# Kernel tuning notes

Measured on AMD Instinct MI355X. Metric: run time of the kernel, lower is better.

Reference implementation:

```python
import jax, jax.numpy as jnp
import numpy as np

B, C, N, K_NN = 16, 64, 2048, 3
OUT_C = 64


def setup_inputs() -> dict:
    key = jax.random.key(0)
    k1, k2, k3 = jax.random.split(key, 3)
    x = jax.random.normal(k1, (B, C, N), dtype=jnp.float32)
    fan_in = C * K_NN
    bound = 1.0 / np.sqrt(fan_in)
    W = jax.random.uniform(k2, (OUT_C, C, K_NN), minval=-bound, maxval=bound, dtype=jnp.float32)
    b = jax.random.uniform(k3, (OUT_C,), minval=-bound, maxval=bound, dtype=jnp.float32)
    return {"x": x, "W": W, "b": b}


def reference(x, W, b):
    # x: [B, C, N]; W: [O, C, K]; b: [O]
    K = W.shape[-1]
    # Pairwise squared distances: dist[b,i,j] = |x_i|^2 + |x_j|^2 - 2 x_i.x_j.
    # The original takes sqrt, but sqrt is monotone and the distances are only
    # used for top-k index selection, so we select on squared distances (same indices).
    norm_sq = jnp.sum(x * x, axis=1)                      # [B, N]
    dot = jnp.einsum('bcn,bcm->bnm', x, x)                # [B, N, N]
    dist_sq = norm_sq[:, :, None] + norm_sq[:, None, :] - 2.0 * dot  # [B, N, N]
    # K smallest distances per row -> neighbor indices [B, N, K]
    _, idx = jax.lax.top_k(-dist_sq, K)
    # Gather neighbors: neigh[b, c, n, k] = x[b, c, idx[b, n, k]]
    neigh = jax.vmap(lambda xb, ib: xb[:, ib])(x, idx)    # [B, C, N, K]
    # Conv1d with kernel_size == stride == K over the flattened [B, C, N*K]
    # tensor is exactly a per-window contraction over the K neighbors.
    out = jnp.einsum('bcnk,ock->bon', neigh, W) + b[None, :, None]  # [B, O, N]
    return out
```

## Files before the change

kernel.cpp:

```cpp
#include <hip/hip_runtime.h>
#include <cfloat>
#include <climits>

#define B_DIM 16
#define C_DIM 64
#define N_DIM 2048
#define O_DIM 64
#define K_NN  3

typedef __attribute__((ext_vector_type(8))) short bf16x8;
typedef __attribute__((ext_vector_type(4))) float floatx4;

#define GLDS16(gsrc, ldst)                                        \
  __builtin_amdgcn_global_load_lds(                               \
      (const __attribute__((address_space(1))) void*)(gsrc),      \
      (__attribute__((address_space(3))) void*)(ldst), 16, 0, 0)

__device__ __forceinline__ unsigned short f32_to_bf16_rne(float f) {
  unsigned int u = __float_as_uint(f);
  return (unsigned short)((u + 0x7fffu + ((u >> 16) & 1u)) >> 16);
}
__device__ __forceinline__ float bf16_to_f32(unsigned short h) {
  return __uint_as_float(((unsigned int)h) << 16);
}

__device__ __forceinline__ unsigned med3u(unsigned a, unsigned b, unsigned c) {
  unsigned mn = min(a, b), mx = max(a, b);
  return max(mn, min(mx, c));
}

__device__ __forceinline__ void ins4p(unsigned u, int jv, unsigned* k, int* j) {
  bool c3 = u < k[3], c2 = u < k[2], c1 = u < k[1], c0 = u < k[0];
  k[3] = c2 ? k[2] : (c3 ? u  : k[3]);
  j[3] = c2 ? j[2] : (c3 ? jv : j[3]);
  k[2] = c1 ? k[1] : (c2 ? u  : k[2]);
  j[2] = c1 ? j[1] : (c2 ? jv : j[2]);
  k[1] = c0 ? k[0] : (c1 ? u  : k[1]);
  j[1] = c0 ? j[0] : (c1 ? jv : j[1]);
  k[0] = c0 ? u  : k[0];
  j[0] = c0 ? jv : j[0];
}

__global__ __launch_bounds__(256) void prep_kernel(
    const float* __restrict__ x, float* __restrict__ xT,
    unsigned short* __restrict__ xTh, unsigned short* __restrict__ xTl,
    double* __restrict__ nd, float* __restrict__ nf,
    const float* __restrict__ W, float* __restrict__ Wt) {
  int bid = blockIdx.x;
  int t = threadIdx.x;
  if (bid >= 512) {
    int t2 = (bid - 512) * 256 + t;
    int o  = t2 / (C_DIM * K_NN);
    int ck = t2 - o * (C_DIM * K_NN);
    Wt[ck * O_DIM + o] = W[t2];
    return;
  }
  __shared__ __align__(16) float xs[C_DIM][68];
  int b  = bid >> 5;
  int n0 = (bid & 31) * 64;
  const float* xb = x + (size_t)b * C_DIM * N_DIM;
  #pragma unroll
  for (int r = 0; r < 4; ++r) {
    int idx = r * 256 + t;
    int c = idx >> 4;
    int qq = idx & 15;
    *(float4*)&xs[c][qq * 4] = *(const float4*)(xb + (size_t)c * N_DIM + n0 + qq * 4);
  }
  __syncthreads();
  int n = t >> 2, cg = t & 3;
  float v[16];
  #pragma unroll
  for (int cc = 0; cc < 16; ++cc) v[cc] = xs[cg * 16 + cc][n];
  double ps = 0.0;
  #pragma unroll
  for (int cc = 0; cc < 16; ++cc) ps = fma((double)v[cc], (double)v[cc], ps);
  ps += __shfl_xor(ps, 1, 64);
  ps += __shfl_xor(ps, 2, 64);
  size_t row = (size_t)b * N_DIM + n0 + n;
  #pragma unroll
  for (int qq = 0; qq < 4; ++qq) {
    float4 wv; wv.x = v[qq*4]; wv.y = v[qq*4+1]; wv.z = v[qq*4+2]; wv.w = v[qq*4+3];
    *(float4*)&xT[row * C_DIM + cg * 16 + qq * 4] = wv;
  }
  unsigned short hh[16], ll[16];
  #pragma unroll
  for (int cc = 0; cc < 16; ++cc) {
    hh[cc] = f32_to_bf16_rne(v[cc]);
    ll[cc] = f32_to_bf16_rne(v[cc] - bf16_to_f32(hh[cc]));
  }
  #pragma unroll
  for (int e = 0; e < 2; ++e) {
    int phys = (2 * cg + e) ^ (n & 7);
    unsigned int hp[4], lp[4];
    #pragma unroll
    for (int xk = 0; xk < 4; ++xk) {
      hp[xk] = (unsigned)hh[e*8 + 2*xk] | ((unsigned)hh[e*8 + 2*xk + 1] << 16);
      lp[xk] = (unsigned)ll[e*8 + 2*xk] | ((unsigned)ll[e*8 + 2*xk + 1] << 16);
    }
    ((uint4*)xTh)[row * 8 + phys] = *(uint4*)hp;
    ((uint4*)xTl)[row * 8 + phys] = *(uint4*)lp;
  }
  if (cg == 0) {
    nd[row] = ps;
    nf[row] = (float)ps + 512.0f;
  }
}

__global__ __launch_bounds__(256, 4) void topk_kernel(
    const unsigned short* __restrict__ xTh, const unsigned short* __restrict__ xTl,
    const float* __restrict__ nf, unsigned short* __restrict__ cand) {
  __shared__ __align__(16) unsigned short Jh[2][64 * 64];
  __shared__ __align__(16) unsigned short Jl[2][64 * 64];
  int bid   = blockIdx.x;
  int q     = bid & 3;
  int itile = (bid >> 2) & 15;
  int b     = bid >> 6;
  int i0    = itile * 128;
  int jq0   = q * 512;
  int t = threadIdx.x;
  int w = t >> 6, lane = t & 63, quad = lane >> 4, col = lane & 15;
  int csw = col & 7;
  const unsigned short* xh = xTh + (size_t)b * N_DIM * 64;
  const unsigned short* xl = xTl + (size_t)b * N_DIM * 64;
  const float* nfb = nf + b * N_DIM;

  bf16x8 ih[2][2], il[2][2];
  #pragma unroll
  for (int s2 = 0; s2 < 2; ++s2) {
    #pragma unroll
    for (int ks = 0; ks < 2; ++ks) {
      size_t row = i0 + w * 32 + s2 * 16 + col;
      int phys = (ks * 4 + quad) ^ csw;
      ih[s2][ks] = *(const bf16x8*)(xh + row * 64 + phys * 8);
      il[s2][ks] = *(const bf16x8*)(xl + row * 64 + phys * 8);
    }
  }

  unsigned ck[2][4];
  #pragma unroll
  for (int s2 = 0; s2 < 2; ++s2)
    ck[s2][0] = ck[s2][1] = ck[s2][2] = ck[s2][3] = 0xFFFFFFFFu;

  int a0 = col * 64 + ((quad ^ csw) * 8);
  int a1 = col * 64 + (((4 + quad) ^ csw) * 8);

  const unsigned short* sbh = xh + (size_t)(jq0 + w * 16) * 64 + lane * 8;
  const unsigned short* sbl = xl + (size_t)(jq0 + w * 16) * 64 + lane * 8;
  int ldsb = w * 16 * 64;

  #pragma unroll
  for (int k2 = 0; k2 < 2; ++k2) {
    GLDS16(sbh + k2 * 512, &Jh[0][ldsb + k2 * 512]);
    GLDS16(sbl + k2 * 512, &Jl[0][ldsb + k2 * 512]);
  }
  __syncthreads();

  #pragma unroll
  for (int js = 0; js < 8; ++js) {
    int cur = js & 1, nxt = cur ^ 1;
    int j0 = jq0 + js * 64;

    if (js < 7) {
      #pragma unroll
      for (int k2 = 0; k2 < 2; ++k2) {
        GLDS16(sbh + (js + 1) * 4096 + k2 * 512, &Jh[nxt][ldsb + k2 * 512]);
        GLDS16(sbl + (js + 1) * 4096 + k2 * 512, &Jl[nxt][ldsb + k2 * 512]);
      }
    }

    floatx4 acc[2][4];
    #pragma unroll
    for (int s2 = 0; s2 < 2; ++s2)
      #pragma unroll
      for (int jt = 0; jt < 4; ++jt) acc[s2][jt] = (floatx4){0.f, 0.f, 0.f, 0.f};

    #pragma unroll
    for (int ks = 0; ks < 2; ++ks) {
      int ab = ks ? a1 : a0;
      #pragma unroll
      for (int jt = 0; jt < 4; ++jt) {
        bf16x8 jh = *(const bf16x8*)&Jh[cur][jt * 1024 + ab];
        bf16x8 jl = *(const bf16x8*)&Jl[cur][jt * 1024 + ab];
        #pragma unroll
        for (int s2 = 0; s2 < 2; ++s2) {
          acc[s2][jt] = __builtin_amdgcn_mfma_f32_16x16x32_bf16(jl, ih[s2][ks], acc[s2][jt], 0, 0, 0);
          acc[s2][jt] = __builtin_amdgcn_mfma_f32_16x16x32_bf16(jh, il[s2][ks], acc[s2][jt], 0, 0, 0);
          acc[s2][jt] = __builtin_amdgcn_mfma_f32_16x16x32_bf16(jh, ih[s2][ks], acc[s2][jt], 0, 0, 0);
        }
      }
    }

    unsigned locb = (unsigned)(js << 4);
    int jb = j0 + quad * 4;
    #pragma unroll
    for (int jt = 0; jt < 4; ++jt) {
      float4 nv = *(const float4*)(nfb + jb + jt * 16);
      float nfa[4] = {nv.x, nv.y, nv.z, nv.w};
      #pragma unroll
      for (int r = 0; r < 4; ++r) {
        unsigned idbits = locb | (unsigned)(jt * 4 + r);
        #pragma unroll
        for (int s2 = 0; s2 < 2; ++s2) {
          float key = fmaf(-2.0f, acc[s2][jt][r], nfa[r]);
          unsigned u = (__float_as_uint(key) & 0xFFFFFF80u) | idbits;
          unsigned m0 = min(ck[s2][0], u);
          unsigned m1 = med3u(ck[s2][0], u, ck[s2][1]);
          unsigned m2 = med3u(ck[s2][1], u, ck[s2][2]);
          unsigned m3 = med3u(ck[s2][2], u, ck[s2][3]);
          ck[s2][0] = m0; ck[s2][1] = m1; ck[s2][2] = m2; ck[s2][3] = m3;
        }
      }
    }

    __syncthreads();
  }

  #pragma unroll
  for (int s2 = 0; s2 < 2; ++s2) {
    int cj[4];
    unsigned cku[4];
    #pragma unroll
    for (int s = 0; s < 4; ++s) {
      unsigned loc = ck[s2][s] & 127u;
      cj[s] = jq0 + (int)((loc >> 4) << 6) + (int)(((loc >> 2) & 3u) << 4) +
              (quad << 2) + (int)(loc & 3u);
      cku[s] = ck[s2][s];
    }
    #pragma unroll
    for (int m = 16; m < 64; m <<= 1) {
      unsigned tu[4]; int tj[4];
      #pragma unroll
      for (int s = 0; s < 4; ++s) {
        tu[s] = __shfl_xor(cku[s], m, 64);
        tj[s] = __shfl_xor(cj[s], m, 64);
      }
      #pragma unroll
      for (int s = 0; s < 4; ++s) ins4p(tu[s], tj[s], cku, cj);
    }
    if (quad == 0) {
      int row = b * N_DIM + i0 + w * 32 + s2 * 16 + col;
      unsigned short* cp = cand + row * 16 + q * 4;
      cp[0] = (unsigned short)cj[0];
      cp[1] = (unsigned short)cj[1];
      cp[2] = (unsigned short)cj[2];
      cp[3] = (unsigned short)cj[3];
    }
  }
}

#define NT   64
#define NPAD 68
__global__ __launch_bounds__(256) void conv_kernel(
    const float* __restrict__ xT, const double* __restrict__ nd,
    const unsigned short* __restrict__ cand,
    const float* __restrict__ Wt, const float* __restrict__ bias,
    float* __restrict__ out) {
  __shared__ __align__(16) float nb[C_DIM * K_NN][NPAD];
  __shared__ unsigned short tks[NT][4];
  int bid = blockIdx.x;
  int b  = bid >> 5;
  int n0 = (bid & 31) * NT;
  const float* xtb = xT + (size_t)b * N_DIM * C_DIM;
  int t = threadIdx.x;
  int w = t >> 6, lane = t & 63;
  int cid = lane >> 2, seg = lane & 3;

  for (int it = 0; it < 16; ++it) {
    int nn = w * 16 + it;
    int row = b * N_DIM + n0 + nn;
    int j = cand[row * 16 + cid];
    const float* xn = xtb + ((size_t)(n0 + nn) * C_DIM) + seg * 16;
    const float* xj = xtb + ((size_t)j * C_DIM) + seg * 16;
    double pd = 0.0;
    #pragma unroll
    for (int qq = 0; qq < 4; ++qq) {
      float4 a  = *(const float4*)(xn + qq * 4);
      float4 bb = *(const float4*)(xj + qq * 4);
      pd = fma((double)a.x, (double)bb.x, pd);
      pd = fma((double)a.y, (double)bb.y, pd);
      pd = fma((double)a.z, (double)bb.z, pd);
      pd = fma((double)a.w, (double)bb.w, pd);
    }
    pd += __shfl_xor(pd, 1, 64);
    pd += __shfl_xor(pd, 2, 64);
    double key = fma(-2.0, pd, nd[b * N_DIM + j] + 512.0);
    unsigned long long u =
        ((unsigned long long)__double_as_longlong(key) & ~2047ull) |
        (unsigned long long)(unsigned)j;
    unsigned long long v = u;
    #pragma unroll
    for (int p = 0; p < 3; ++p) {
      unsigned long long m = v;
      #pragma unroll
      for (int msk = 4; msk < 64; msk <<= 1) {
        unsigned long long o = __shfl_xor(m, msk, 64);
        m = (o < m) ? o : m;
      }
      if (lane == 0) tks[nn][p] = (unsigned short)(m & 2047ull);
      v = (v == m) ? ~0ull : v;
    }
  }
  __syncthreads();

  #pragma unroll
  for (int p = 0; p < 12; ++p) {
    int u = p * 256 + t;
    int sg = u & 15;
    int r  = u >> 4;
    int k = r >> 6, n = r & 63;
    int j = tks[n][k];
    float4 v = *(const float4*)(xtb + (size_t)j * C_DIM + sg * 4);
    nb[(sg * 4 + 0) * 3 + k][n] = v.x;
    nb[(sg * 4 + 1) * 3 + k][n] = v.y;
    nb[(sg * 4 + 2) * 3 + k][n] = v.z;
    nb[(sg * 4 + 3) * 3 + k][n] = v.w;
  }
  __syncthreads();

  int ng = t & 15, og = t >> 4;
  float acc[4][4];
  #pragma unroll
  for (int oo = 0; oo < 4; ++oo) {
    float bv = bias[(og << 2) + oo];
    #pragma unroll
    for (int nn2 = 0; nn2 < 4; ++nn2) acc[oo][nn2] = bv;
  }
  const float* nbp = &nb[0][0] + (ng << 2);
  const float* wtp = Wt + (og << 2);
  #pragma unroll 4
  for (int ckk = 0; ckk < C_DIM * K_NN; ++ckk) {
    float4 nv = *(const float4*)(nbp + ckk * NPAD);
    float4 wv = *(const float4*)(wtp + ckk * O_DIM);
    float na[4] = {nv.x, nv.y, nv.z, nv.w};
    float wa[4] = {wv.x, wv.y, wv.z, wv.w};
    #pragma unroll
    for (int oo = 0; oo < 4; ++oo)
      #pragma unroll
      for (int nn2 = 0; nn2 < 4; ++nn2)
        acc[oo][nn2] = fmaf(wa[oo], na[nn2], acc[oo][nn2]);
  }
  #pragma unroll
  for (int oo = 0; oo < 4; ++oo) {
    int o = (og << 2) + oo;
    float4 v; v.x = acc[oo][0]; v.y = acc[oo][1]; v.z = acc[oo][2]; v.w = acc[oo][3];
    *(float4*)&out[(size_t)(b * O_DIM + o) * N_DIM + n0 + (ng << 2)] = v;
  }
}

extern "C" void kernel_launch(void* const* d_in, const int* in_sizes, int n_in,
                              void* d_out, int out_size, void* d_ws, size_t ws_size,
                              hipStream_t stream) {
  const float* x    = (const float*)d_in[0];
  const float* W    = (const float*)d_in[1];
  const float* bias = (const float*)d_in[2];
  float* out = (float*)d_out;
  char* ws = (char*)d_ws;
  float*          xT  = (float*)ws;
  unsigned short* xTh = (unsigned short*)(ws + 8388608);
  unsigned short* xTl = (unsigned short*)(ws + 12582912);
  double*         nd  = (double*)(ws + 16777216);
  float*          nfp = (float*)(ws + 17039360);
  unsigned short* cd  = (unsigned short*)(ws + 17170432);
  float*          Wt  = (float*)(ws + 18219008);

  prep_kernel<<<512 + 48, 256, 0, stream>>>(x, xT, xTh, xTl, nd, nfp, W, Wt);
  topk_kernel<<<B_DIM * 16 * 4, 256, 0, stream>>>(xTh, xTl, nfp, cd);
  conv_kernel<<<B_DIM * (N_DIM / NT), 256, 0, stream>>>(xT, nd, cd, Wt, bias, out);
}
```

Measured before the change: 144.6 us.

## Shrink conv tile to 16 points per block for more blocks

```diff
diff --git a/kernel.cpp b/kernel.cpp
--- a/kernel.cpp
+++ b/kernel.cpp
@@ -248,9 +248,9 @@
   }
 }
 
-#define NT   64
-#define NPAD 68
-__global__ __launch_bounds__(256) void conv_kernel(
+#define NT   16
+#define NPAD 20
+__global__ __launch_bounds__(256, 6) void conv_kernel(
     const float* __restrict__ xT, const double* __restrict__ nd,
     const unsigned short* __restrict__ cand,
     const float* __restrict__ Wt, const float* __restrict__ bias,
@@ -258,15 +258,15 @@
   __shared__ __align__(16) float nb[C_DIM * K_NN][NPAD];
   __shared__ unsigned short tks[NT][4];
   int bid = blockIdx.x;
-  int b  = bid >> 5;
-  int n0 = (bid & 31) * NT;
+  int b  = bid >> 7;
+  int n0 = (bid & 127) * NT;
   const float* xtb = xT + (size_t)b * N_DIM * C_DIM;
   int t = threadIdx.x;
   int w = t >> 6, lane = t & 63;
   int cid = lane >> 2, seg = lane & 3;
 
-  for (int it = 0; it < 16; ++it) {
-    int nn = w * 16 + it;
+  for (int it = 0; it < 4; ++it) {
+    int nn = w * 4 + it;
     int row = b * N_DIM + n0 + nn;
     int j = cand[row * 16 + cid];
     const float* xn = xtb + ((size_t)(n0 + nn) * C_DIM) + seg * 16;
@@ -303,11 +303,12 @@
   __syncthreads();
 
   #pragma unroll
-  for (int p = 0; p < 12; ++p) {
+  for (int p = 0; p < 3; ++p) {
     int u = p * 256 + t;
-    int sg = u & 15;
-    int r  = u >> 4;
-    int k = r >> 6, n = r & 63;
+    int n  = u & 15;
+    int h  = u >> 4;
+    int k  = h >> 4;
+    int sg = h & 15;
     int j = tks[n][k];
     float4 v = *(const float4*)(xtb + (size_t)j * C_DIM + sg * 4);
     nb[(sg * 4 + 0) * 3 + k][n] = v.x;
@@ -317,34 +318,26 @@
   }
   __syncthreads();
 
-  int ng = t & 15, og = t >> 4;
-  float acc[4][4];
-  #pragma unroll
-  for (int oo = 0; oo < 4; ++oo) {
-    float bv = bias[(og << 2) + oo];
-    #pragma unroll
-    for (int nn2 = 0; nn2 < 4; ++nn2) acc[oo][nn2] = bv;
+  int ng = t & 3, og = t >> 2;
+  float acc[4];
+  {
+    float bv = bias[og];
+    #pragma unroll
+    for (int nn2 = 0; nn2 < 4; ++nn2) acc[nn2] = bv;
   }
   const float* nbp = &nb[0][0] + (ng << 2);
-  const float* wtp = Wt + (og << 2);
-  #pragma unroll 4
+  const float* wtp = Wt + og;
+  #pragma unroll 8
   for (int ckk = 0; ckk < C_DIM * K_NN; ++ckk) {
     float4 nv = *(const float4*)(nbp + ckk * NPAD);
-    float4 wv = *(const float4*)(wtp + ckk * O_DIM);
-    float na[4] = {nv.x, nv.y, nv.z, nv.w};
-    float wa[4] = {wv.x, wv.y, wv.z, wv.w};
-    #pragma unroll
-    for (int oo = 0; oo < 4; ++oo)
-      #pragma unroll
-      for (int nn2 = 0; nn2 < 4; ++nn2)
-        acc[oo][nn2] = fmaf(wa[oo], na[nn2], acc[oo][nn2]);
-  }
-  #pragma unroll
-  for (int oo = 0; oo < 4; ++oo) {
-    int o = (og << 2) + oo;
-    float4 v; v.x = acc[oo][0]; v.y = acc[oo][1]; v.z = acc[oo][2]; v.w = acc[oo][3];
-    *(float4*)&out[(size_t)(b * O_DIM + o) * N_DIM + n0 + (ng << 2)] = v;
-  }
+    float wv = wtp[ckk * O_DIM];
+    acc[0] = fmaf(wv, nv.x, acc[0]);
+    acc[1] = fmaf(wv, nv.y, acc[1]);
+    acc[2] = fmaf(wv, nv.z, acc[2]);
+    acc[3] = fmaf(wv, nv.w, acc[3]);
+  }
+  float4 v; v.x = acc[0]; v.y = acc[1]; v.z = acc[2]; v.w = acc[3];
+  *(float4*)&out[(size_t)(b * O_DIM + og) * N_DIM + n0 + (ng << 2)] = v;
 }
 
 extern "C" void kernel_launch(void* const* d_in, const int* in_sizes, int n_in,
```

After: 140.5 us. -2.8%, faster.

## Split exact top-k refinement into separate kernel and remap block order by XCD

Applied to the files above, without the earlier changes.

```diff
diff --git a/kernel.cpp b/kernel.cpp
--- a/kernel.cpp
+++ b/kernel.cpp
@@ -112,6 +112,7 @@
   __shared__ __align__(16) unsigned short Jh[2][64 * 64];
   __shared__ __align__(16) unsigned short Jl[2][64 * 64];
   int bid   = blockIdx.x;
+  bid = (bid & 7) * 128 + (bid >> 3);
   int q     = bid & 3;
   int itile = (bid >> 2) & 15;
   int b     = bid >> 6;
@@ -248,72 +249,91 @@
   }
 }
 
+#define RNT 16
+__global__ __launch_bounds__(256, 4) void refine_kernel(
+    const float* __restrict__ xT, const double* __restrict__ nd,
+    const unsigned short* __restrict__ cand,
+    unsigned long long* __restrict__ tks_g) {
+  __shared__ unsigned long long keys[RNT][17];
+  int bid = blockIdx.x;
+  bid = (bid & 7) * 256 + (bid >> 3);
+  int b  = bid >> 7;
+  int n0 = (bid & 127) * RNT;
+  int t = threadIdx.x;
+  int row = t >> 4, c = t & 15;
+  int nn = n0 + row;
+  int j = cand[(b * N_DIM + nn) * 16 + c];
+  const float* xtb = xT + (size_t)b * N_DIM * C_DIM;
+  const float* xn = xtb + (size_t)nn * C_DIM;
+  const float* xj = xtb + (size_t)j * C_DIM;
+  double nj = nd[b * N_DIM + j];
+
+  double p[4];
+  #pragma unroll
+  for (int qq = 0; qq < 4; ++qq) {
+    double s = 0.0;
+    #pragma unroll
+    for (int r = 0; r < 4; ++r) {
+      float4 a  = *(const float4*)(xn + qq * 16 + r * 4);
+      float4 bb = *(const float4*)(xj + qq * 16 + r * 4);
+      s = fma((double)a.x, (double)bb.x, s);
+      s = fma((double)a.y, (double)bb.y, s);
+      s = fma((double)a.z, (double)bb.z, s);
+      s = fma((double)a.w, (double)bb.w, s);
+    }
+    p[qq] = s;
+  }
+  double pd = (p[0] + p[1]) + (p[2] + p[3]);
+  double key = fma(-2.0, pd, nj + 512.0);
+  unsigned long long u =
+      ((unsigned long long)__double_as_longlong(key) & ~2047ull) |
+      (unsigned long long)(unsigned)j;
+  keys[row][c] = u;
+  __syncthreads();
+
+  if (t < RNT) {
+    unsigned long long k0 = ~0ull, k1 = ~0ull, k2 = ~0ull;
+    #pragma unroll
+    for (int s = 0; s < 16; ++s) {
+      unsigned long long v = keys[t][s];
+      bool c0 = v < k0, c1 = v < k1, c2 = v < k2;
+      k2 = c1 ? k1 : (c2 ? v : k2);
+      k1 = c0 ? k0 : (c1 ? v : k1);
+      k0 = c0 ? v : k0;
+    }
+    tks_g[b * N_DIM + n0 + t] =
+        (k0 & 2047ull) | ((k1 & 2047ull) << 16) | ((k2 & 2047ull) << 32);
+  }
+}
+
 #define NT   64
 #define NPAD 68
-__global__ __launch_bounds__(256) void conv_kernel(
-    const float* __restrict__ xT, const double* __restrict__ nd,
-    const unsigned short* __restrict__ cand,
+__global__ __launch_bounds__(256, 2) void conv_kernel(
+    const float* __restrict__ xT, const unsigned long long* __restrict__ tks_g,
     const float* __restrict__ Wt, const float* __restrict__ bias,
     float* __restrict__ out) {
   __shared__ __align__(16) float nb[C_DIM * K_NN][NPAD];
-  __shared__ unsigned short tks[NT][4];
   int bid = blockIdx.x;
+  bid = (bid & 7) * 64 + (bid >> 3);
   int b  = bid >> 5;
   int n0 = (bid & 31) * NT;
   const float* xtb = xT + (size_t)b * N_DIM * C_DIM;
   int t = threadIdx.x;
   int w = t >> 6, lane = t & 63;
-  int cid = lane >> 2, seg = lane & 3;
-
-  for (int it = 0; it < 16; ++it) {
-    int nn = w * 16 + it;
-    int row = b * N_DIM + n0 + nn;
-    int j = cand[row * 16 + cid];
-    const float* xn = xtb + ((size_t)(n0 + nn) * C_DIM) + seg * 16;
-    const float* xj = xtb + ((size_t)j * C_DIM) + seg * 16;
-    double pd = 0.0;
-    #pragma unroll
-    for (int qq = 0; qq < 4; ++qq) {
-      float4 a  = *(const float4*)(xn + qq * 4);
-      float4 bb = *(const float4*)(xj + qq * 4);
-      pd = fma((double)a.x, (double)bb.x, pd);
-      pd = fma((double)a.y, (double)bb.y, pd);
-      pd = fma((double)a.z, (double)bb.z, pd);
-      pd = fma((double)a.w, (double)bb.w, pd);
-    }
-    pd += __shfl_xor(pd, 1, 64);
-    pd += __shfl_xor(pd, 2, 64);
-    double key = fma(-2.0, pd, nd[b * N_DIM + j] + 512.0);
-    unsigned long long u =
-        ((unsigned long long)__double_as_longlong(key) & ~2047ull) |
-        (unsigned long long)(unsigned)j;
-    unsigned long long v = u;
-    #pragma unroll
-    for (int p = 0; p < 3; ++p) {
-      unsigned long long m = v;
-      #pragma unroll
-      for (int msk = 4; msk < 64; msk <<= 1) {
-        unsigned long long o = __shfl_xor(m, msk, 64);
-        m = (o < m) ? o : m;
-      }
-      if (lane == 0) tks[nn][p] = (unsigned short)(m & 2047ull);
-      v = (v == m) ? ~0ull : v;
-    }
-  }
-  __syncthreads();
+
+  unsigned long long t3 = tks_g[b * N_DIM + n0 + lane];
 
   #pragma unroll
   for (int p = 0; p < 12; ++p) {
-    int u = p * 256 + t;
-    int sg = u & 15;
-    int r  = u >> 4;
-    int k = r >> 6, n = r & 63;
-    int j = tks[n][k];
+    int h  = p * 4 + w;
+    int k  = h >> 4;
+    int sg = h & 15;
+    int j = (int)((t3 >> (16 * k)) & 2047ull);
     float4 v = *(const float4*)(xtb + (size_t)j * C_DIM + sg * 4);
-    nb[(sg * 4 + 0) * 3 + k][n] = v.x;
-    nb[(sg * 4 + 1) * 3 + k][n] = v.y;
-    nb[(sg * 4 + 2) * 3 + k][n] = v.z;
-    nb[(sg * 4 + 3) * 3 + k][n] = v.w;
+    nb[(sg * 4 + 0) * 3 + k][lane] = v.x;
+    nb[(sg * 4 + 1) * 3 + k][lane] = v.y;
+    nb[(sg * 4 + 2) * 3 + k][lane] = v.z;
+    nb[(sg * 4 + 3) * 3 + k][lane] = v.w;
   }
   __syncthreads();
 
@@ -362,8 +382,10 @@
   float*          nfp = (float*)(ws + 17039360);
   unsigned short* cd  = (unsigned short*)(ws + 17170432);
   float*          Wt  = (float*)(ws + 18219008);
+  unsigned long long* tks = (unsigned long long*)(ws + 8388608);
 
   prep_kernel<<<512 + 48, 256, 0, stream>>>(x, xT, xTh, xTl, nd, nfp, W, Wt);
   topk_kernel<<<B_DIM * 16 * 4, 256, 0, stream>>>(xTh, xTl, nfp, cd);
-  conv_kernel<<<B_DIM * (N_DIM / NT), 256, 0, stream>>>(xT, nd, cd, Wt, bias, out);
-}
+  refine_kernel<<<B_DIM * (N_DIM / RNT), 256, 0, stream>>>(xT, nd, cd, tks);
+  conv_kernel<<<B_DIM * (N_DIM / NT), 256, 0, stream>>>(xT, tks, Wt, bias, out);
+}
```

Result: slower. 149.6 us (+3.5%).

## Restructure conv candidate rescoring and swizzle block order in both kernels

Applied to the files above, without the earlier changes.

```diff
diff --git a/kernel.cpp b/kernel.cpp
--- a/kernel.cpp
+++ b/kernel.cpp
@@ -112,6 +112,7 @@
   __shared__ __align__(16) unsigned short Jh[2][64 * 64];
   __shared__ __align__(16) unsigned short Jl[2][64 * 64];
   int bid   = blockIdx.x;
+  bid = (bid & 7) * 128 + (bid >> 3);
   int q     = bid & 3;
   int itile = (bid >> 2) & 15;
   int b     = bid >> 6;
@@ -211,7 +212,6 @@
         }
       }
     }
-
     __syncthreads();
   }
 
@@ -250,55 +250,69 @@
 
 #define NT   64
 #define NPAD 68
-__global__ __launch_bounds__(256) void conv_kernel(
+__global__ __launch_bounds__(256, 3) void conv_kernel(
     const float* __restrict__ xT, const double* __restrict__ nd,
     const unsigned short* __restrict__ cand,
     const float* __restrict__ Wt, const float* __restrict__ bias,
     float* __restrict__ out) {
-  __shared__ __align__(16) float nb[C_DIM * K_NN][NPAD];
-  __shared__ unsigned short tks[NT][4];
+  __shared__ __align__(16) char smem[C_DIM * K_NN * NPAD * 4];
+  __shared__ __align__(16) unsigned long long tks[NT];
+  float (*nb)[NPAD] = (float (*)[NPAD])smem;
+  unsigned long long (*keys)[17] = (unsigned long long (*)[17])smem;
+  unsigned short* cjs = (unsigned short*)(smem + 8704);
+
   int bid = blockIdx.x;
+  bid = (bid & 7) * 64 + (bid >> 3);
   int b  = bid >> 5;
   int n0 = (bid & 31) * NT;
   const float* xtb = xT + (size_t)b * N_DIM * C_DIM;
+  const double* ndb = nd + b * N_DIM;
   int t = threadIdx.x;
-  int w = t >> 6, lane = t & 63;
-  int cid = lane >> 2, seg = lane & 3;
-
-  for (int it = 0; it < 16; ++it) {
-    int nn = w * 16 + it;
-    int row = b * N_DIM + n0 + nn;
-    int j = cand[row * 16 + cid];
-    const float* xn = xtb + ((size_t)(n0 + nn) * C_DIM) + seg * 16;
-    const float* xj = xtb + ((size_t)j * C_DIM) + seg * 16;
+  int w = t >> 6, lane = t & 63, quad = lane >> 4, ql = lane & 15;
+
+  if (t < 128) {
+    ((uint4*)cjs)[t] =
+        ((const uint4*)(cand + ((size_t)b * N_DIM + n0) * 16))[t];
+  }
+  __syncthreads();
+
+  #pragma unroll 8
+  for (int s = 0; s < 64; ++s) {
+    int rowl = w * 16 + (s >> 2);
+    int c = (s & 3) * 4 + quad;
+    int j = cjs[rowl * 16 + c];
+    const float* xn = xtb + (size_t)(n0 + rowl) * C_DIM + ql * 4;
+    const float* xj = xtb + (size_t)j * C_DIM + ql * 4;
+    float4 a  = *(const float4*)xn;
+    float4 bb = *(const float4*)xj;
     double pd = 0.0;
-    #pragma unroll
-    for (int qq = 0; qq < 4; ++qq) {
-      float4 a  = *(const float4*)(xn + qq * 4);
-      float4 bb = *(const float4*)(xj + qq * 4);
-      pd = fma((double)a.x, (double)bb.x, pd);
-      pd = fma((double)a.y, (double)bb.y, pd);
-      pd = fma((double)a.z, (double)bb.z, pd);
-      pd = fma((double)a.w, (double)bb.w, pd);
-    }
+    pd = fma((double)a.x, (double)bb.x, pd);
+    pd = fma((double)a.y, (double)bb.y, pd);
+    pd = fma((double)a.z, (double)bb.z, pd);
+    pd = fma((double)a.w, (double)bb.w, pd);
     pd += __shfl_xor(pd, 1, 64);
     pd += __shfl_xor(pd, 2, 64);
-    double key = fma(-2.0, pd, nd[b * N_DIM + j] + 512.0);
+    pd += __shfl_xor(pd, 4, 64);
+    pd += __shfl_xor(pd, 8, 64);
+    double key = fma(-2.0, pd, ndb[j] + 512.0);
     unsigned long long u =
         ((unsigned long long)__double_as_longlong(key) & ~2047ull) |
         (unsigned long long)(unsigned)j;
-    unsigned long long v = u;
-    #pragma unroll
-    for (int p = 0; p < 3; ++p) {
-      unsigned long long m = v;
-      #pragma unroll
-      for (int msk = 4; msk < 64; msk <<= 1) {
-        unsigned long long o = __shfl_xor(m, msk, 64);
-        m = (o < m) ? o : m;
-      }
-      if (lane == 0) tks[nn][p] = (unsigned short)(m & 2047ull);
-      v = (v == m) ? ~0ull : v;
-    }
+    if (ql == 0) keys[rowl][c] = u;
+  }
+  __syncthreads();
+
+  if (t < NT) {
+    unsigned long long k0 = ~0ull, k1 = ~0ull, k2 = ~0ull;
+    #pragma unroll
+    for (int s = 0; s < 16; ++s) {
+      unsigned long long v = keys[t][s];
+      bool c0 = v < k0, c1 = v < k1, c2 = v < k2;
+      k2 = c1 ? k1 : (c2 ? v : k2);
+      k1 = c0 ? k0 : (c1 ? v : k1);
+      k0 = c0 ? v : k0;
+    }
+    tks[t] = (k0 & 2047ull) | ((k1 & 2047ull) << 16) | ((k2 & 2047ull) << 32);
   }
   __syncthreads();
 
@@ -308,7 +322,7 @@
     int sg = u & 15;
     int r  = u >> 4;
     int k = r >> 6, n = r & 63;
-    int j = tks[n][k];
+    int j = (int)((tks[n] >> (16 * k)) & 2047ull);
     float4 v = *(const float4*)(xtb + (size_t)j * C_DIM + sg * 4);
     nb[(sg * 4 + 0) * 3 + k][n] = v.x;
     nb[(sg * 4 + 1) * 3 + k][n] = v.y;
```

Result: slower. 154.9 us (+7.1%).
